# Kernel optimization log

Hardware: AMD Instinct MI355X
Metric: run time of the kernel (lower is better)

The kernel has to match this reference:

```python
import jax, jax.numpy as jnp
import numpy as np

DIM = 2048
SEQ = 8192
NUM_HEADS = 16
PROJ_DIM = DIM // 4  # proj_ratio = 4.0
EPS = 1e-5


def setup_inputs() -> dict:
    key = jax.random.key(0)
    ks = jax.random.split(key, 8)
    s = 0.02  # param init scale
    return {
        "x": jax.random.normal(ks[0], (SEQ, DIM), jnp.float32),
        "q": jax.random.normal(ks[1], (1, DIM), jnp.float32),
        "W_kv": jax.random.normal(ks[2], (2 * DIM, DIM), jnp.float32) * s,
        "b_kv": jax.random.normal(ks[3], (2 * DIM,), jnp.float32) * s,
        "W_p1": jax.random.normal(ks[4], (PROJ_DIM, DIM), jnp.float32) * s,
        "b_p1": jax.random.normal(ks[5], (PROJ_DIM,), jnp.float32) * s,
        "W_p2": jax.random.normal(ks[6], (DIM, PROJ_DIM), jnp.float32) * s,
        "b_p2": jax.random.normal(ks[7], (DIM,), jnp.float32) * s,
        "ln_w": jnp.ones((PROJ_DIM,), jnp.float32),
        "ln_b": jnp.zeros((PROJ_DIM,), jnp.float32),
    }


def reference(x, q, W_kv, b_kv, W_p1, b_p1, W_p2, b_p2, ln_w, ln_b):
    seq, dim = x.shape
    h = NUM_HEADS
    d = dim // h

    # kv projection: [s, 2*dim]; split '(n h d)' with n leading -> k = first dim cols
    kv = x @ W_kv.T + b_kv
    k = kv[:, :dim].reshape(seq, h, d).transpose(1, 0, 2)   # [h, s, d]
    v = kv[:, dim:].reshape(seq, h, d).transpose(1, 0, 2)   # [h, s, d]
    qh = q.reshape(h, 1, d)                                  # '1 (h d) -> h 1 d'

    # single-query attention (qk_norm=False -> Identity norms)
    attn = jnp.einsum('hqd,hkd->hqk', qh, k) / jnp.sqrt(jnp.asarray(d, x.dtype))
    attn = jax.nn.softmax(attn, axis=-1)                     # [h, 1, s]
    x1 = jnp.einsum('hqk,hkd->hqd', attn, v)                 # [h, 1, d]
    x1 = x1.transpose(1, 0, 2).reshape(1, dim)               # 'h s d -> s (h d)'

    # proj MLP: proj1 -> LayerNorm -> relu -> proj2
    h1 = x1 @ W_p1.T + b_p1                                  # [1, proj_dim]
    mu = jnp.mean(h1, axis=-1, keepdims=True)
    var = jnp.mean(jnp.square(h1 - mu), axis=-1, keepdims=True)
    h1 = (h1 - mu) / jnp.sqrt(var + EPS) * ln_w + ln_b
    x1 = jax.nn.relu(h1) @ W_p2.T + b_p2                     # [1, dim]

    # residual broadcast: [s, dim] + [1, dim]
    return x + x1
```

## Files before the change

### kernel.cpp

```cpp
#include <hip/hip_runtime.h>
#include <math.h>

#define SEQ   8192
#define DIM   2048
#define NH    16
#define DH    128
#define PD    512

static constexpr float LN_EPS = 1e-5f;
static constexpr float SCALE  = 0.08838834764831845f;

typedef __bf16 bf16x8 __attribute__((ext_vector_type(8)));
typedef float  f32x4  __attribute__((ext_vector_type(4)));

static constexpr size_t OFF_QB   = 0;
static constexpr size_t OFF_SMP  = 16;
static constexpr size_t OFF_QWB  = 528;
static constexpr size_t OFF_PCTX = 16912;
static constexpr size_t OFF_CTX  = OFF_PCTX + 8388608;
static constexpr size_t OFF_X1   = OFF_CTX + 32768;
static constexpr size_t OFF_H1R  = OFF_X1 + 2048;
static constexpr size_t OFF_X1F  = OFF_H1R + 512;

__global__ __launch_bounds__(256) void k_prep(const float* __restrict__ q,
                                              const float* __restrict__ Wkv,
                                              const float* __restrict__ bkv,
                                              __bf16* __restrict__ qWb,
                                              float* __restrict__ qb,
                                              float* __restrict__ smp) {
    int t = threadIdx.x;
    int h = blockIdx.x >> 4, jc = blockIdx.x & 15;
    int col = t & 127, kh = t >> 7;
    int j = jc * 128 + col;
    const float* w  = Wkv + (size_t)(h * DH + kh * 64) * DIM + j;
    const float* qh = q + h * DH + kh * 64;
    float acc = 0.f;
#pragma unroll 16
    for (int d = 0; d < 64; ++d)
        acc += qh[d] * __builtin_nontemporal_load(w + (size_t)d * DIM);
    __shared__ float part[128];
    if (kh) part[col] = acc;
    __syncthreads();
    if (!kh) qWb[h * DIM + j] = (__bf16)(acc + part[col]);
    if (jc == 0 && t < 64) {
        float p = q[h*DH + t] * bkv[h*DH + t] + q[h*DH + 64 + t] * bkv[h*DH + 64 + t];
        for (int off = 32; off; off >>= 1) p += __shfl_down(p, off);
        if (t == 0) qb[h] = p;
    }
    if (blockIdx.x == 0) { smp[t] = 0.f; smp[t + 256] = 0.f; }
}

__global__ __launch_bounds__(512) void k_fctx(const float* __restrict__ x,
                                              const __bf16* __restrict__ qWb,
                                              const float* __restrict__ qb,
                                              float* __restrict__ pctx,
                                              float* __restrict__ smp) {
    const int b = blockIdx.x, t = threadIdx.x;
    const int w8 = t >> 6, lane = t & 63;
    const int s0 = b * 32;
    const int rg = w8 & 1, kq = w8 >> 1;
    const int r = lane & 15, quad = lane >> 4;

    __shared__ float dpart[2][4][64][4];
    __shared__ float att[32][NH];
    __shared__ float hsum[NH];
    if (t < NH) hsum[t] = 0.f;

    const float*  xrow = x + (size_t)(s0 + rg * 16 + r) * DIM + quad * 8;
    const __bf16* brow = qWb + r * DIM + quad * 8;
    const int kbase = kq * 512;

    bf16x8 WV[16];
#pragma unroll
    for (int i = 0; i < 16; ++i)
        WV[i] = *(const bf16x8*)(brow + kbase + i * 32);
    float4 XA[16], XB[16];
#pragma unroll
    for (int i = 0; i < 16; ++i) {
        XA[i] = *(const float4*)(xrow + kbase + i * 32);
        XB[i] = *(const float4*)(xrow + kbase + i * 32 + 4);
    }
    __builtin_amdgcn_sched_barrier(0);

    f32x4 acc = {0.f, 0.f, 0.f, 0.f};
#pragma unroll
    for (int i = 0; i < 16; ++i) {
        bf16x8 af;
        af[0] = (__bf16)XA[i].x; af[1] = (__bf16)XA[i].y;
        af[2] = (__bf16)XA[i].z; af[3] = (__bf16)XA[i].w;
        af[4] = (__bf16)XB[i].x; af[5] = (__bf16)XB[i].y;
        af[6] = (__bf16)XB[i].z; af[7] = (__bf16)XB[i].w;
        acc = __builtin_amdgcn_mfma_f32_16x16x32_bf16(af, WV[i], acc, 0, 0, 0);
    }
    *(f32x4*)&dpart[rg][kq][lane][0] = acc;
    __syncthreads();

    {
        const int h = t & 15, slp = t >> 4;
        const int rg2 = slp >> 4, sli = slp & 15;
        const int quad2 = sli >> 2, reg2 = sli & 3;
        const int lane2 = quad2 * 16 + h;
        float v = dpart[rg2][0][lane2][reg2] + dpart[rg2][1][lane2][reg2]
                + dpart[rg2][2][lane2][reg2] + dpart[rg2][3][lane2][reg2];
        float e = __expf((v + qb[h]) * SCALE);
        att[slp][h] = e;
        atomicAdd(&hsum[h], e);
    }
    __syncthreads();
    if (t < NH) atomicAdd(&smp[t * 32 + (b & 31)], hsum[t]);

    const int j0 = t * 4;
    f32x4 zero = {0.f, 0.f, 0.f, 0.f};
    f32x4 acc4[NH];
#pragma unroll
    for (int h = 0; h < NH; ++h) acc4[h] = zero;
#pragma unroll 4
    for (int rr = 0; rr < 32; ++rr) {
        f32x4 xv = *(const f32x4*)(x + (size_t)(s0 + rr) * DIM + j0);
        const f32x4* ar = (const f32x4*)att[rr];
        f32x4 a0 = ar[0], a1 = ar[1], a2 = ar[2], a3 = ar[3];
        float aa[16];
        *(f32x4*)&aa[0] = a0; *(f32x4*)&aa[4]  = a1;
        *(f32x4*)&aa[8] = a2; *(f32x4*)&aa[12] = a3;
#pragma unroll
        for (int h = 0; h < NH; ++h) acc4[h] += xv * aa[h];
    }
#pragma unroll
    for (int h = 0; h < NH; ++h)
        __builtin_nontemporal_store(acc4[h],
            (f32x4*)&pctx[((size_t)(b * NH + h)) * DIM + j0]);
}

__global__ __launch_bounds__(256) void k_ctxred(const float* __restrict__ pctx,
                                                const float* __restrict__ smp,
                                                float* __restrict__ ctx) {
    const int b = blockIdx.x, t = threadIdx.x;
    const int h = b >> 5;
    const int col = t & 63, ch = t >> 6;
    __shared__ float sInv;
    __shared__ float psum[4][64];
    const size_t idx = (size_t)b * 64 + col;
    const int c0 = ch * 64;
    float s = 0.f;
#pragma unroll 16
    for (int c = 0; c < 64; ++c)
        s += __builtin_nontemporal_load(&pctx[(size_t)(c0 + c) * (NH * DIM) + idx]);
    psum[ch][col] = s;
    if (t < 32) {
        float v = smp[h * 32 + t];
        for (int off = 16; off; off >>= 1) v += __shfl_xor(v, off);
        if (t == 0) sInv = 1.0f / v;
    }
    __syncthreads();
    if (ch == 0)
        ctx[idx] = (psum[0][col] + psum[1][col] + psum[2][col] + psum[3][col]) * sInv;
}

__global__ __launch_bounds__(256) void k_x1(const float* __restrict__ Wkv,
                                            const float* __restrict__ bkv,
                                            const float* __restrict__ ctx,
                                            float* __restrict__ x1) {
    int row = blockIdx.x * 4 + (threadIdx.x >> 6);
    int lane = threadIdx.x & 63;
    const float* w = Wkv + (size_t)(DIM + row) * DIM;
    const float* c = ctx + (row >> 7) * DIM;
    float acc = 0.f;
#pragma unroll
    for (int k = 0; k < 8; ++k) {
        int j = k * 256 + lane * 4;
        f32x4 wv = __builtin_nontemporal_load((const f32x4*)&w[j]);
        f32x4 cv = *(const f32x4*)&c[j];
        acc += wv[0]*cv[0] + wv[1]*cv[1] + wv[2]*cv[2] + wv[3]*cv[3];
    }
    for (int off = 32; off; off >>= 1) acc += __shfl_xor(acc, off);
    if (lane == 0) x1[row] = acc + bkv[DIM + row];
}

__global__ __launch_bounds__(256) void k_h1(const float* __restrict__ Wp1,
                                            const float* __restrict__ bp1,
                                            const float* __restrict__ x1,
                                            float* __restrict__ h1raw) {
    int row = blockIdx.x * 4 + (threadIdx.x >> 6);
    int lane = threadIdx.x & 63;
    const float* w = Wp1 + (size_t)row * DIM;
    float acc = 0.f;
#pragma unroll
    for (int k = 0; k < 8; ++k) {
        int j = k * 256 + lane * 4;
        f32x4 wv = __builtin_nontemporal_load((const f32x4*)&w[j]);
        f32x4 cv = *(const f32x4*)&x1[j];
        acc += wv[0]*cv[0] + wv[1]*cv[1] + wv[2]*cv[2] + wv[3]*cv[3];
    }
    for (int off = 32; off; off >>= 1) acc += __shfl_xor(acc, off);
    if (lane == 0) h1raw[row] = acc + bp1[row];
}

__global__ __launch_bounds__(256) void k_x1f(const float* __restrict__ Wp2,
                                             const float* __restrict__ bp2,
                                             const float* __restrict__ h1raw,
                                             const float* __restrict__ lnw,
                                             const float* __restrict__ lnb,
                                             float* __restrict__ x1f) {
    int row = blockIdx.x * 4 + (threadIdx.x >> 6);
    int lane = threadIdx.x & 63;
    int j = lane * 8;
    float4 va = *(const float4*)&h1raw[j];
    float4 vb = *(const float4*)&h1raw[j + 4];
    float s = va.x + va.y + va.z + va.w + vb.x + vb.y + vb.z + vb.w;
    for (int off = 32; off; off >>= 1) s += __shfl_xor(s, off);
    float mu = s * (1.0f / PD);
    float dx[8];
    dx[0]=va.x-mu; dx[1]=va.y-mu; dx[2]=va.z-mu; dx[3]=va.w-mu;
    dx[4]=vb.x-mu; dx[5]=vb.y-mu; dx[6]=vb.z-mu; dx[7]=vb.w-mu;
    float s2 = 0.f;
#pragma unroll
    for (int i = 0; i < 8; ++i) s2 += dx[i] * dx[i];
    for (int off = 32; off; off >>= 1) s2 += __shfl_xor(s2, off);
    float rstd = rsqrtf(s2 * (1.0f / PD) + LN_EPS);
    float4 lw0 = *(const float4*)&lnw[j], lw1 = *(const float4*)&lnw[j + 4];
    float4 lb0 = *(const float4*)&lnb[j], lb1 = *(const float4*)&lnb[j + 4];
    float hln[8];
    hln[0]=fmaxf(dx[0]*rstd*lw0.x+lb0.x,0.f); hln[1]=fmaxf(dx[1]*rstd*lw0.y+lb0.y,0.f);
    hln[2]=fmaxf(dx[2]*rstd*lw0.z+lb0.z,0.f); hln[3]=fmaxf(dx[3]*rstd*lw0.w+lb0.w,0.f);
    hln[4]=fmaxf(dx[4]*rstd*lw1.x+lb1.x,0.f); hln[5]=fmaxf(dx[5]*rstd*lw1.y+lb1.y,0.f);
    hln[6]=fmaxf(dx[6]*rstd*lw1.z+lb1.z,0.f); hln[7]=fmaxf(dx[7]*rstd*lw1.w+lb1.w,0.f);
    const float* w = Wp2 + (size_t)row * PD + j;
    f32x4 w0 = __builtin_nontemporal_load((const f32x4*)w);
    f32x4 w1 = __builtin_nontemporal_load((const f32x4*)(w + 4));
    float acc = w0[0]*hln[0] + w0[1]*hln[1] + w0[2]*hln[2] + w0[3]*hln[3]
              + w1[0]*hln[4] + w1[1]*hln[5] + w1[2]*hln[6] + w1[3]*hln[7];
    for (int off = 32; off; off >>= 1) acc += __shfl_xor(acc, off);
    if (lane == 0) x1f[row] = acc + bp2[row];
}

__global__ __launch_bounds__(256) void k_out(const float* __restrict__ x,
                                             const float* __restrict__ x1f,
                                             float* __restrict__ out) {
    size_t i = (size_t)blockIdx.x * 512 + threadIdx.x;
    f32x4 xv = ((const f32x4*)x)[i];
    f32x4 a  = ((const f32x4*)x1f)[(int)(i & 511)];
    __builtin_nontemporal_store(xv + a, (f32x4*)out + i);
    size_t i2 = i + 256;
    f32x4 xv2 = ((const f32x4*)x)[i2];
    f32x4 a2  = ((const f32x4*)x1f)[(int)(i2 & 511)];
    __builtin_nontemporal_store(xv2 + a2, (f32x4*)out + i2);
}

extern "C" void kernel_launch(void* const* d_in, const int* in_sizes, int n_in,
                              void* d_out, int out_size, void* d_ws, size_t ws_size,
                              hipStream_t stream) {
    const float* x    = (const float*)d_in[0];
    const float* q    = (const float*)d_in[1];
    const float* Wkv  = (const float*)d_in[2];
    const float* bkv  = (const float*)d_in[3];
    const float* Wp1  = (const float*)d_in[4];
    const float* bp1  = (const float*)d_in[5];
    const float* Wp2  = (const float*)d_in[6];
    const float* bp2  = (const float*)d_in[7];
    const float* lnw  = (const float*)d_in[8];
    const float* lnb  = (const float*)d_in[9];
    float* out = (float*)d_out;
    float* ws  = (float*)d_ws;

    float*  qb    = ws + OFF_QB;
    float*  smp   = ws + OFF_SMP;
    __bf16* qWb   = (__bf16*)(ws + OFF_QWB);
    float*  pctx  = ws + OFF_PCTX;
    float*  ctx   = ws + OFF_CTX;
    float*  x1    = ws + OFF_X1;
    float*  h1raw = ws + OFF_H1R;
    float*  x1f   = ws + OFF_X1F;

    k_prep  <<<256, 256, 0, stream>>>(q, Wkv, bkv, qWb, qb, smp);
    k_fctx  <<<256, 512, 0, stream>>>(x, qWb, qb, pctx, smp);
    k_ctxred<<<512, 256, 0, stream>>>(pctx, smp, ctx);
    k_x1    <<<512, 256, 0, stream>>>(Wkv, bkv, ctx, x1);
    k_h1    <<<128, 256, 0, stream>>>(Wp1, bp1, x1, h1raw);
    k_x1f   <<<512, 256, 0, stream>>>(Wp2, bp2, h1raw, lnw, lnb, x1f);
    k_out   <<<8192, 256, 0, stream>>>(x, x1f, out);
}
```

Baseline: 208.9 us.

## Stage x tiles in LDS via direct global-to-LDS loads in fused context kernel

The fused score/context kernel now copies each 16-row chunk of x into shared memory with global_load_lds, then reuses that copy for both the bf16 MFMA score computation and the attention-weighted context accumulation. The 32-row block is processed in two halves. This removes the second global read of x that the context loop used to issue. In exchange it uses about 131 KB of LDS per block, which limits occupancy to one block per CU. It also serializes the load, score and context phases behind barriers, with no overlap between loading and compute.

```diff
diff --git a/kernel.cpp b/kernel.cpp
--- a/kernel.cpp
+++ b/kernel.cpp
@@ -21,6 +21,13 @@
 static constexpr size_t OFF_X1   = OFF_CTX + 32768;
 static constexpr size_t OFF_H1R  = OFF_X1 + 2048;
 static constexpr size_t OFF_X1F  = OFF_H1R + 512;
+
+__device__ __forceinline__ void gload_lds16(const float* g, float* l) {
+    __builtin_amdgcn_global_load_lds(
+        (const __attribute__((address_space(1))) uint32_t*)g,
+        (__attribute__((address_space(3))) uint32_t*)l,
+        16, 0, 0);
+}
 
 __global__ __launch_bounds__(256) void k_prep(const float* __restrict__ q,
                                               const float* __restrict__ Wkv,
@@ -50,6 +57,7 @@
     if (blockIdx.x == 0) { smp[t] = 0.f; smp[t + 256] = 0.f; }
 }
 
+#define ROWF 2052
 __global__ __launch_bounds__(512) void k_fctx(const float* __restrict__ x,
                                               const __bf16* __restrict__ qWb,
                                               const float* __restrict__ qb,
@@ -58,78 +66,85 @@
     const int b = blockIdx.x, t = threadIdx.x;
     const int w8 = t >> 6, lane = t & 63;
     const int s0 = b * 32;
-    const int rg = w8 & 1, kq = w8 >> 1;
     const int r = lane & 15, quad = lane >> 4;
 
-    __shared__ float dpart[2][4][64][4];
-    __shared__ float att[32][NH];
+    __shared__ float ldsx[16 * ROWF];
+    __shared__ float dpart[8][64][4];
+    __shared__ float att[16][NH];
     __shared__ float hsum[NH];
     if (t < NH) hsum[t] = 0.f;
 
-    const float*  xrow = x + (size_t)(s0 + rg * 16 + r) * DIM + quad * 8;
-    const __bf16* brow = qWb + r * DIM + quad * 8;
-    const int kbase = kq * 512;
-
-    bf16x8 WV[16];
-#pragma unroll
-    for (int i = 0; i < 16; ++i)
-        WV[i] = *(const bf16x8*)(brow + kbase + i * 32);
-    float4 XA[16], XB[16];
-#pragma unroll
-    for (int i = 0; i < 16; ++i) {
-        XA[i] = *(const float4*)(xrow + kbase + i * 32);
-        XB[i] = *(const float4*)(xrow + kbase + i * 32 + 4);
-    }
-    __builtin_amdgcn_sched_barrier(0);
-
-    f32x4 acc = {0.f, 0.f, 0.f, 0.f};
-#pragma unroll
-    for (int i = 0; i < 16; ++i) {
-        bf16x8 af;
-        af[0] = (__bf16)XA[i].x; af[1] = (__bf16)XA[i].y;
-        af[2] = (__bf16)XA[i].z; af[3] = (__bf16)XA[i].w;
-        af[4] = (__bf16)XB[i].x; af[5] = (__bf16)XB[i].y;
-        af[6] = (__bf16)XB[i].z; af[7] = (__bf16)XB[i].w;
-        acc = __builtin_amdgcn_mfma_f32_16x16x32_bf16(af, WV[i], acc, 0, 0, 0);
-    }
-    *(f32x4*)&dpart[rg][kq][lane][0] = acc;
-    __syncthreads();
-
-    {
-        const int h = t & 15, slp = t >> 4;
-        const int rg2 = slp >> 4, sli = slp & 15;
-        const int quad2 = sli >> 2, reg2 = sli & 3;
-        const int lane2 = quad2 * 16 + h;
-        float v = dpart[rg2][0][lane2][reg2] + dpart[rg2][1][lane2][reg2]
-                + dpart[rg2][2][lane2][reg2] + dpart[rg2][3][lane2][reg2];
-        float e = __expf((v + qb[h]) * SCALE);
-        att[slp][h] = e;
-        atomicAdd(&hsum[h], e);
-    }
-    __syncthreads();
+    const int kbase = w8 * 256;
+    const int j0 = t * 4;
+    f32x4 acc4[NH];
+#pragma unroll
+    for (int h = 0; h < NH; ++h) acc4[h] = (f32x4){0.f, 0.f, 0.f, 0.f};
+
+    for (int h2 = 0; h2 < 2; ++h2) {
+        if (h2) __syncthreads();
+        {
+            const float* gsrc = x + (size_t)(s0 + h2 * 16) * DIM + kbase + lane * 4;
+            float*       ldst = ldsx + kbase + lane * 4;
+#pragma unroll
+            for (int i = 0; i < 16; ++i)
+                gload_lds16(gsrc + (size_t)i * DIM, ldst + i * ROWF);
+        }
+        asm volatile("s_waitcnt vmcnt(0)" ::: "memory");
+        __syncthreads();
+
+        {
+            const __bf16* brow = qWb + r * DIM + kbase + quad * 8;
+            const float*  lrow = ldsx + r * ROWF + kbase + quad * 8;
+            f32x4 acc = {0.f, 0.f, 0.f, 0.f};
+#pragma unroll
+            for (int i = 0; i < 8; ++i) {
+                f32x4 xa = *(const f32x4*)(lrow + i * 32);
+                f32x4 xb = *(const f32x4*)(lrow + i * 32 + 4);
+                bf16x8 af;
+                af[0] = (__bf16)xa[0]; af[1] = (__bf16)xa[1];
+                af[2] = (__bf16)xa[2]; af[3] = (__bf16)xa[3];
+                af[4] = (__bf16)xb[0]; af[5] = (__bf16)xb[1];
+                af[6] = (__bf16)xb[2]; af[7] = (__bf16)xb[3];
+                bf16x8 bv = *(const bf16x8*)(brow + i * 32);
+                acc = __builtin_amdgcn_mfma_f32_16x16x32_bf16(af, bv, acc, 0, 0, 0);
+            }
+            *(f32x4*)&dpart[w8][lane][0] = acc;
+        }
+        __syncthreads();
+
+        if (t < 256) {
+            const int h = t & 15, sl = t >> 4;
+            const int quad2 = sl >> 2, reg2 = sl & 3;
+            const int lane2 = quad2 * 16 + h;
+            float v = 0.f;
+#pragma unroll
+            for (int kk = 0; kk < 8; ++kk) v += dpart[kk][lane2][reg2];
+            float e = __expf((v + qb[h]) * SCALE);
+            att[sl][h] = e;
+            atomicAdd(&hsum[h], e);
+        }
+        __syncthreads();
+
+#pragma unroll 4
+        for (int rr = 0; rr < 16; ++rr) {
+            f32x4 xv = *(const f32x4*)(ldsx + rr * ROWF + j0);
+            const f32x4* ar = (const f32x4*)att[rr];
+            f32x4 a0 = ar[0], a1 = ar[1], a2 = ar[2], a3 = ar[3];
+            float aa[16];
+            *(f32x4*)&aa[0] = a0; *(f32x4*)&aa[4]  = a1;
+            *(f32x4*)&aa[8] = a2; *(f32x4*)&aa[12] = a3;
+#pragma unroll
+            for (int h = 0; h < NH; ++h) acc4[h] += xv * aa[h];
+        }
+    }
+
     if (t < NH) atomicAdd(&smp[t * 32 + (b & 31)], hsum[t]);
-
-    const int j0 = t * 4;
-    f32x4 zero = {0.f, 0.f, 0.f, 0.f};
-    f32x4 acc4[NH];
-#pragma unroll
-    for (int h = 0; h < NH; ++h) acc4[h] = zero;
-#pragma unroll 4
-    for (int rr = 0; rr < 32; ++rr) {
-        f32x4 xv = *(const f32x4*)(x + (size_t)(s0 + rr) * DIM + j0);
-        const f32x4* ar = (const f32x4*)att[rr];
-        f32x4 a0 = ar[0], a1 = ar[1], a2 = ar[2], a3 = ar[3];
-        float aa[16];
-        *(f32x4*)&aa[0] = a0; *(f32x4*)&aa[4]  = a1;
-        *(f32x4*)&aa[8] = a2; *(f32x4*)&aa[12] = a3;
-#pragma unroll
-        for (int h = 0; h < NH; ++h) acc4[h] += xv * aa[h];
-    }
 #pragma unroll
     for (int h = 0; h < NH; ++h)
         __builtin_nontemporal_store(acc4[h],
             (f32x4*)&pctx[((size_t)(b * NH + h)) * DIM + j0]);
 }
+#undef ROWF
 
 __global__ __launch_bounds__(256) void k_ctxred(const float* __restrict__ pctx,
                                                 const float* __restrict__ smp,
```

New measurement: 206.7 us. Within noise of the previous version (-1.1%).

## Split fused logits/context kernel into separate logits and weighted-context passes

Applied to the files above, without the earlier changes.

Replaces the fused k_fctx kernel with two kernels. The first computes exp-logits for 16-row tiles and writes them to a workspace buffer. The second computes weighted partial contexts over 128-row chunks and 256 columns, storing 64 partials per head instead of 256. This shrinks the partial-context buffer and the later reduction, and raises parallelism in the logits pass. In exchange, x is read twice from memory and one extra launch plus a logits round-trip is added.

```diff
diff --git a/kernel.cpp b/kernel.cpp
--- a/kernel.cpp
+++ b/kernel.cpp
@@ -16,8 +16,9 @@
 static constexpr size_t OFF_QB   = 0;
 static constexpr size_t OFF_SMP  = 16;
 static constexpr size_t OFF_QWB  = 528;
-static constexpr size_t OFF_PCTX = 16912;
-static constexpr size_t OFF_CTX  = OFF_PCTX + 8388608;
+static constexpr size_t OFF_ELOG = 16912;
+static constexpr size_t OFF_PCTX = OFF_ELOG + 131072;
+static constexpr size_t OFF_CTX  = OFF_PCTX + 2097152;
 static constexpr size_t OFF_X1   = OFF_CTX + 32768;
 static constexpr size_t OFF_H1R  = OFF_X1 + 2048;
 static constexpr size_t OFF_X1F  = OFF_H1R + 512;
@@ -50,85 +51,88 @@
     if (blockIdx.x == 0) { smp[t] = 0.f; smp[t + 256] = 0.f; }
 }
 
-__global__ __launch_bounds__(512) void k_fctx(const float* __restrict__ x,
-                                              const __bf16* __restrict__ qWb,
-                                              const float* __restrict__ qb,
-                                              float* __restrict__ pctx,
-                                              float* __restrict__ smp) {
-    const int b = blockIdx.x, t = threadIdx.x;
-    const int w8 = t >> 6, lane = t & 63;
-    const int s0 = b * 32;
-    const int rg = w8 & 1, kq = w8 >> 1;
+__global__ __launch_bounds__(256) void k_logits(const float* __restrict__ x,
+                                                const __bf16* __restrict__ qWb,
+                                                const float* __restrict__ qb,
+                                                float* __restrict__ elogT,
+                                                float* __restrict__ smp) {
+    const int t = threadIdx.x;
+    const int w = t >> 6, lane = t & 63;
     const int r = lane & 15, quad = lane >> 4;
-
-    __shared__ float dpart[2][4][64][4];
-    __shared__ float att[32][NH];
+    const int s0 = blockIdx.x * 16;
+    __shared__ float dpart[4][64][4];
     __shared__ float hsum[NH];
     if (t < NH) hsum[t] = 0.f;
 
-    const float*  xrow = x + (size_t)(s0 + rg * 16 + r) * DIM + quad * 8;
+    const float*  xrow = x + (size_t)(s0 + r) * DIM + quad * 8;
     const __bf16* brow = qWb + r * DIM + quad * 8;
-    const int kbase = kq * 512;
-
-    bf16x8 WV[16];
-#pragma unroll
-    for (int i = 0; i < 16; ++i)
-        WV[i] = *(const bf16x8*)(brow + kbase + i * 32);
-    float4 XA[16], XB[16];
-#pragma unroll
+    const int kbase = w * 512;
+
+    f32x4 acc = {0.f, 0.f, 0.f, 0.f};
+#pragma unroll 4
     for (int i = 0; i < 16; ++i) {
-        XA[i] = *(const float4*)(xrow + kbase + i * 32);
-        XB[i] = *(const float4*)(xrow + kbase + i * 32 + 4);
-    }
-    __builtin_amdgcn_sched_barrier(0);
-
-    f32x4 acc = {0.f, 0.f, 0.f, 0.f};
-#pragma unroll
-    for (int i = 0; i < 16; ++i) {
+        int k = kbase + i * 32;
+        float4 xa = *(const float4*)(xrow + k);
+        float4 xb = *(const float4*)(xrow + k + 4);
         bf16x8 af;
-        af[0] = (__bf16)XA[i].x; af[1] = (__bf16)XA[i].y;
-        af[2] = (__bf16)XA[i].z; af[3] = (__bf16)XA[i].w;
-        af[4] = (__bf16)XB[i].x; af[5] = (__bf16)XB[i].y;
-        af[6] = (__bf16)XB[i].z; af[7] = (__bf16)XB[i].w;
-        acc = __builtin_amdgcn_mfma_f32_16x16x32_bf16(af, WV[i], acc, 0, 0, 0);
-    }
-    *(f32x4*)&dpart[rg][kq][lane][0] = acc;
+        af[0] = (__bf16)xa.x; af[1] = (__bf16)xa.y;
+        af[2] = (__bf16)xa.z; af[3] = (__bf16)xa.w;
+        af[4] = (__bf16)xb.x; af[5] = (__bf16)xb.y;
+        af[6] = (__bf16)xb.z; af[7] = (__bf16)xb.w;
+        bf16x8 bf = *(const bf16x8*)(brow + k);
+        acc = __builtin_amdgcn_mfma_f32_16x16x32_bf16(af, bf, acc, 0, 0, 0);
+    }
+    dpart[w][lane][0] = acc[0];
+    dpart[w][lane][1] = acc[1];
+    dpart[w][lane][2] = acc[2];
+    dpart[w][lane][3] = acc[3];
     __syncthreads();
 
     {
-        const int h = t & 15, slp = t >> 4;
-        const int rg2 = slp >> 4, sli = slp & 15;
-        const int quad2 = sli >> 2, reg2 = sli & 3;
-        const int lane2 = quad2 * 16 + h;
-        float v = dpart[rg2][0][lane2][reg2] + dpart[rg2][1][lane2][reg2]
-                + dpart[rg2][2][lane2][reg2] + dpart[rg2][3][lane2][reg2];
+        const int lane2 = t & 63, reg = t >> 6;
+        const int h = lane2 & 15, sl = (lane2 >> 4) * 4 + reg;
+        float v = dpart[0][lane2][reg] + dpart[1][lane2][reg]
+                + dpart[2][lane2][reg] + dpart[3][lane2][reg];
         float e = __expf((v + qb[h]) * SCALE);
-        att[slp][h] = e;
+        elogT[(size_t)(s0 + sl) * NH + h] = e;
         atomicAdd(&hsum[h], e);
     }
     __syncthreads();
-    if (t < NH) atomicAdd(&smp[t * 32 + (b & 31)], hsum[t]);
-
-    const int j0 = t * 4;
-    f32x4 zero = {0.f, 0.f, 0.f, 0.f};
-    f32x4 acc4[NH];
-#pragma unroll
-    for (int h = 0; h < NH; ++h) acc4[h] = zero;
+    if (t < NH) atomicAdd(&smp[t * 32 + (blockIdx.x & 31)], hsum[t]);
+}
+
+__global__ __launch_bounds__(256) void k_wctx(const float* __restrict__ x,
+                                              const float* __restrict__ elogT,
+                                              float* __restrict__ pctx) {
+    const int b = blockIdx.x, t = threadIdx.x;
+    const int sc = b >> 3, jc = b & 7;
+    const int s0 = sc * 128;
+    const int j = jc * 256 + t;
+
+    __shared__ float att[128 * NH];
+    for (int i = t; i < 128 * NH; i += 256)
+        att[i] = elogT[(size_t)s0 * NH + i];
+    __syncthreads();
+
+    float acc[NH];
+#pragma unroll
+    for (int h = 0; h < NH; ++h) acc[h] = 0.f;
+    const float* xp = x + (size_t)s0 * DIM + j;
 #pragma unroll 4
-    for (int rr = 0; rr < 32; ++rr) {
-        f32x4 xv = *(const f32x4*)(x + (size_t)(s0 + rr) * DIM + j0);
-        const f32x4* ar = (const f32x4*)att[rr];
+    for (int rr = 0; rr < 128; ++rr) {
+        float xv = xp[(size_t)rr * DIM];
+        const f32x4* ar = (const f32x4*)(att + rr * NH);
         f32x4 a0 = ar[0], a1 = ar[1], a2 = ar[2], a3 = ar[3];
-        float aa[16];
+        float aa[NH];
         *(f32x4*)&aa[0] = a0; *(f32x4*)&aa[4]  = a1;
         *(f32x4*)&aa[8] = a2; *(f32x4*)&aa[12] = a3;
 #pragma unroll
-        for (int h = 0; h < NH; ++h) acc4[h] += xv * aa[h];
+        for (int h = 0; h < NH; ++h) acc[h] += xv * aa[h];
     }
 #pragma unroll
     for (int h = 0; h < NH; ++h)
-        __builtin_nontemporal_store(acc4[h],
-            (f32x4*)&pctx[((size_t)(b * NH + h)) * DIM + j0]);
+        __builtin_nontemporal_store(acc[h],
+            &pctx[((size_t)(sc * NH + h)) * DIM + j]);
 }
 
 __global__ __launch_bounds__(256) void k_ctxred(const float* __restrict__ pctx,
@@ -140,11 +144,11 @@
     __shared__ float sInv;
     __shared__ float psum[4][64];
     const size_t idx = (size_t)b * 64 + col;
-    const int c0 = ch * 64;
     float s = 0.f;
-#pragma unroll 16
-    for (int c = 0; c < 64; ++c)
-        s += __builtin_nontemporal_load(&pctx[(size_t)(c0 + c) * (NH * DIM) + idx]);
+#pragma unroll
+    for (int i = 0; i < 16; ++i)
+        s += __builtin_nontemporal_load(
+                 &pctx[(size_t)(ch * 16 + i) * (NH * DIM) + idx]);
     psum[ch][col] = s;
     if (t < 32) {
         float v = smp[h * 32 + t];
@@ -265,6 +269,7 @@
     float*  qb    = ws + OFF_QB;
     float*  smp   = ws + OFF_SMP;
     __bf16* qWb   = (__bf16*)(ws + OFF_QWB);
+    float*  elogT = ws + OFF_ELOG;
     float*  pctx  = ws + OFF_PCTX;
     float*  ctx   = ws + OFF_CTX;
     float*  x1    = ws + OFF_X1;
@@ -272,7 +277,8 @@
     float*  x1f   = ws + OFF_X1F;
 
     k_prep  <<<256, 256, 0, stream>>>(q, Wkv, bkv, qWb, qb, smp);
-    k_fctx  <<<256, 512, 0, stream>>>(x, qWb, qb, pctx, smp);
+    k_logits<<<512, 256, 0, stream>>>(x, qWb, qb, elogT, smp);
+    k_wctx  <<<512, 256, 0, stream>>>(x, elogT, pctx);
     k_ctxred<<<512, 256, 0, stream>>>(pctx, smp, ctx);
     k_x1    <<<512, 256, 0, stream>>>(Wkv, bkv, ctx, x1);
     k_h1    <<<128, 256, 0, stream>>>(Wp1, bp1, x1, h1raw);
```

Result: slower. 214.2 us (+2.5%).
